# Performance work log

Hardware: AMD Instinct MI355X
Metric: run time of the kernel (lower is better)

Reference implementation:

```python
import jax, jax.numpy as jnp
import numpy as np

B, T, Q, K, H = 8, 128, 64, 64, 4  # batch, agents, q_dim, kv_dim, heads; neighbors n = T-1


def setup_inputs() -> dict:
    key = jax.random.key(0)
    ks = jax.random.split(key, 9)
    s = 0.05
    return {
        "q_x": jax.random.normal(ks[0], (B, T, Q), dtype=jnp.float32),
        "kv_x": jax.random.normal(ks[1], (B, T, T - 1, K), dtype=jnp.float32),
        # nn.Linear weights stored (out_features, in_features), y = x @ W.T + b
        "Wk": jax.random.normal(ks[2], (H * K, K), dtype=jnp.float32) * s,      # tokeys (no bias)
        "Wq": jax.random.normal(ks[3], (H * K, Q), dtype=jnp.float32) * s,      # toqueries (no bias)
        "Wv": jax.random.normal(ks[4], (H * K, K + Q), dtype=jnp.float32) * s,  # tovalues
        "bv": jax.random.normal(ks[5], (H * K,), dtype=jnp.float32) * s,
        "bias": jax.random.uniform(ks[6], (K,), dtype=jnp.float32, minval=-0.1, maxval=0.1),
        "ws": jax.random.normal(ks[7], (K,), dtype=jnp.float32) * s,            # score_proj weight (1, K) -> (K,)
        "bs": jax.random.normal(ks[8], (), dtype=jnp.float32) * s,              # score_proj bias
    }


def reference(q_x, kv_x, Wk, Wq, Wv, bv, bias, ws, bs):
    b, t, n, k = kv_x.shape            # n = t - 1 neighbors
    q = q_x.shape[-1]
    h = Wk.shape[0] // k
    # key / query projections
    keys = jnp.einsum('btnk,ok->btno', kv_x, Wk).reshape(b, t, n, h, k)
    queries = jnp.einsum('btq,oq->bto', q_x, Wq).reshape(b, t, 1, h, k)
    # additive (Bahdanau) score: linear(tanh(keys + queries + bias)) -> scalar per (b,t,n,h)
    score = jnp.einsum('btnhk,k->btnh', jnp.tanh(keys + queries + bias), ws) + bs
    # values from concat(kv, broadcast query features)
    q_exp = jnp.broadcast_to(q_x[:, :, None, :], (b, t, n, q))
    value_input = jnp.concatenate([kv_x, q_exp], axis=-1)      # (b,t,n,k+q)
    values = (jnp.einsum('btnc,oc->btno', value_input, Wv) + bv).reshape(b, t, n, h, k)
    # softmax over neighbors, weighted sum of values
    w = jax.nn.softmax(score, axis=2)                          # (b,t,n,h)
    x = jnp.einsum('btnh,btnhk->bthk', w, values).reshape(b, t, h * k)
    return x
```

## Files before the change

### kernel.cpp

```cpp
#include <hip/hip_runtime.h>
#include <hip/hip_bf16.h>

#define NB 127
#define SCALE 2.885390081777927f

typedef __attribute__((ext_vector_type(8))) short bf16x8;
typedef __attribute__((ext_vector_type(4))) float f32x4;

#define WKP_S  0
#define WVP_S  16384
#define WQP_S  32768
#define WVQP_S 49152
#define WS_NEEDED ((size_t)(4 * 16384 * 2))

__device__ __forceinline__ short bfs(float f) {
  __hip_bfloat16 h = __float2bfloat16(f);
  return __builtin_bit_cast(short, h);
}
__device__ __forceinline__ unsigned packbf2(float a, float b) {
  unsigned lo = (unsigned short)bfs(a);
  unsigned hi = (unsigned short)bfs(b);
  return lo | (hi << 16);
}
__device__ __forceinline__ float b2f(short s) {
  unsigned u = ((unsigned)(unsigned short)s) << 16;
  return __builtin_bit_cast(float, u);
}
__device__ __forceinline__ bf16x8 gath_s(const float* __restrict__ p, float s) {
  float4 a = *(const float4*)p;
  float4 b = *(const float4*)(p + 4);
  bf16x8 f;
  f[0] = bfs(a.x * s); f[1] = bfs(a.y * s); f[2] = bfs(a.z * s); f[3] = bfs(a.w * s);
  f[4] = bfs(b.x * s); f[5] = bfs(b.y * s); f[6] = bfs(b.z * s); f[7] = bfs(b.w * s);
  return f;
}
__device__ __forceinline__ float sigt(float x) {
  return __builtin_amdgcn_rcpf(__builtin_amdgcn_exp2f(x) + 1.f);
}

__global__ __launch_bounds__(256, 2) void
pack_kernel(const float* __restrict__ Wk, const float* __restrict__ Wq,
            const float* __restrict__ Wv, short* __restrict__ dstall)
{
  const int blk = blockIdx.x;
  const int tid = threadIdx.x;
  const int m = blk >> 4, sub = blk & 15;
  const float* src; int stride, off, dsto; float scl;
  if (m == 0)      { src = Wk; stride = 64;  off = 0;  dsto = WKP_S;  scl = SCALE; }
  else if (m == 1) { src = Wv; stride = 128; off = 0;  dsto = WVP_S;  scl = 1.f; }
  else if (m == 2) { src = Wq; stride = 64;  off = 0;  dsto = WQP_S;  scl = SCALE; }
  else             { src = Wv; stride = 128; off = 64; dsto = WVQP_S; scl = 1.f; }
  short* dst = dstall + dsto;
  int i4 = sub * 256 + tid;
  int o = i4 >> 4, c4 = i4 & 15;
  float4 v = ((const float4*)(src + o * stride + off))[c4];
  int k0 = c4 * 4;
  int kt = k0 >> 5, gg = (k0 & 31) >> 3, j0 = k0 & 7;
  int head = o >> 6, nt = (o >> 4) & 3, ol = o & 15;
  int di = ((((head * 4 + nt) * 2 + kt) * 64) + gg * 16 + ol) * 8 + j0;
  *(uint2*)(dst + di) = make_uint2(packbf2(v.x * scl, v.y * scl),
                                   packbf2(v.z * scl, v.w * scl));
}

template <int PREP>
__global__ __launch_bounds__(256, 2) void
rnn_attn_kernel(const float* __restrict__ q_x, const float* __restrict__ kv_x,
                const float* __restrict__ Wk, const float* __restrict__ Wq,
                const float* __restrict__ Wv, const float* __restrict__ bv,
                const float* __restrict__ bias, const float* __restrict__ wsc,
                const short* __restrict__ pack, float* __restrict__ out)
{
  __shared__ __align__(16) unsigned char Atile[128 * 128];
  __shared__ float4 qv_lds[4][4][4];

  const int tid = threadIdx.x;
  const int bt = blockIdx.x;
  const int lane = tid & 63;
  const int head = tid >> 6;
  const int l15 = lane & 15;
  const int g = lane >> 4;

  const float* kv = kv_x + (size_t)bt * (NB * 64);
  #pragma unroll
  for (int i = 0; i < 8; ++i) {
    int idx = i * 256 + tid;
    int row = idx >> 4, c = idx & 15;
    float4 v = (row < NB) ? ((const float4*)kv)[idx] : make_float4(0.f, 0.f, 0.f, 0.f);
    int byte = (row << 7) + (c << 3);
    byte ^= ((row & 7) << 4);
    *(uint2*)(&Atile[byte]) = make_uint2(packbf2(v.x, v.y), packbf2(v.z, v.w));
  }

  f32x4 qq[4];
  {
    bf16x8 qf0 = gath_s(q_x + bt * 64 + g * 8, 1.f);
    bf16x8 qf1 = gath_s(q_x + bt * 64 + 32 + g * 8, 1.f);
    #pragma unroll
    for (int nt = 0; nt < 4; ++nt) {
      bf16x8 wv0, wv1;
      if (PREP) {
        const bf16x8* pv = (const bf16x8*)(pack + WVQP_S);
        wv0 = pv[((head * 4 + nt) * 2 + 0) * 64 + lane];
        wv1 = pv[((head * 4 + nt) * 2 + 1) * 64 + lane];
      } else {
        int o = head * 64 + nt * 16 + l15;
        wv0 = gath_s(Wv + o * 128 + 64 + g * 8, 1.f);
        wv1 = gath_s(Wv + o * 128 + 64 + 32 + g * 8, 1.f);
      }
      float4 bv4 = ((const float4*)(bv + head * 64))[nt * 4 + g];
      f32x4 b = (f32x4){bv4.x, bv4.y, bv4.z, bv4.w};
      b = __builtin_amdgcn_mfma_f32_16x16x32_bf16(wv0, qf0, b, 0, 0, 0);
      b = __builtin_amdgcn_mfma_f32_16x16x32_bf16(wv1, qf1, b, 0, 0, 0);
      if (l15 == 0) qv_lds[head][nt][g] = make_float4(b[0], b[1], b[2], b[3]);
    }
    #pragma unroll
    for (int nt = 0; nt < 4; ++nt) {
      bf16x8 wq0, wq1;
      if (PREP) {
        const bf16x8* pw = (const bf16x8*)(pack + WQP_S);
        wq0 = pw[((head * 4 + nt) * 2 + 0) * 64 + lane];
        wq1 = pw[((head * 4 + nt) * 2 + 1) * 64 + lane];
      } else {
        int o = head * 64 + nt * 16 + l15;
        wq0 = gath_s(Wq + o * 64 + g * 8, SCALE);
        wq1 = gath_s(Wq + o * 64 + 32 + g * 8, SCALE);
      }
      float4 bs4 = ((const float4*)bias)[nt * 4 + g];
      f32x4 a = (f32x4){bs4.x * SCALE, bs4.y * SCALE, bs4.z * SCALE, bs4.w * SCALE};
      a = __builtin_amdgcn_mfma_f32_16x16x32_bf16(wq0, qf0, a, 0, 0, 0);
      a = __builtin_amdgcn_mfma_f32_16x16x32_bf16(wq1, qf1, a, 0, 0, 0);
      qq[nt] = a;
    }
  }

  f32x4 ws4[4];
  bf16x8 bk[4][2];
  #pragma unroll
  for (int nt = 0; nt < 4; ++nt) {
    float4 t = ((const float4*)wsc)[nt * 4 + g];
    ws4[nt] = (f32x4){-2.f * t.x, -2.f * t.y, -2.f * t.z, -2.f * t.w};
    if (PREP) {
      const bf16x8* pw = (const bf16x8*)(pack + WKP_S);
      bk[nt][0] = pw[((head * 4 + nt) * 2 + 0) * 64 + lane];
      bk[nt][1] = pw[((head * 4 + nt) * 2 + 1) * 64 + lane];
    } else {
      int o = head * 64 + nt * 16 + l15;
      bk[nt][0] = gath_s(Wk + o * 64 + g * 8, SCALE);
      bk[nt][1] = gath_s(Wk + o * 64 + 32 + g * 8, SCALE);
    }
  }

  __syncthreads();

  float pvp0[8], pvp1[8], z = 0.f;
  #pragma unroll
  for (int j = 0; j < 8; ++j) { pvp0[j] = 0.f; pvp1[j] = 0.f; }
  #pragma unroll 1
  for (int mt = 0; mt < 8; ++mt) {
    int row = mt * 16 + l15;
    int byte0 = (row << 7) + g * 16;
    int swz = (l15 & 7) << 4;
    bf16x8 a0 = *(const bf16x8*)(&Atile[byte0 ^ swz]);
    bf16x8 a1 = *(const bf16x8*)(&Atile[(byte0 + 64) ^ swz]);
    float pp0, pp1, pp2, pp3;
    {
      f32x4 acc = qq[0];
      acc = __builtin_amdgcn_mfma_f32_16x16x32_bf16(bk[0][0], a0, acc, 0, 0, 0);
      acc = __builtin_amdgcn_mfma_f32_16x16x32_bf16(bk[0][1], a1, acc, 0, 0, 0);
      pp0 = ws4[0][0] * sigt(acc[0]);
      pp0 = fmaf(ws4[0][1], sigt(acc[1]), pp0);
      pp0 = fmaf(ws4[0][2], sigt(acc[2]), pp0);
      pp0 = fmaf(ws4[0][3], sigt(acc[3]), pp0);
    }
    {
      f32x4 acc = qq[1];
      acc = __builtin_amdgcn_mfma_f32_16x16x32_bf16(bk[1][0], a0, acc, 0, 0, 0);
      acc = __builtin_amdgcn_mfma_f32_16x16x32_bf16(bk[1][1], a1, acc, 0, 0, 0);
      pp1 = ws4[1][0] * sigt(acc[0]);
      pp1 = fmaf(ws4[1][1], sigt(acc[1]), pp1);
      pp1 = fmaf(ws4[1][2], sigt(acc[2]), pp1);
      pp1 = fmaf(ws4[1][3], sigt(acc[3]), pp1);
    }
    {
      f32x4 acc = qq[2];
      acc = __builtin_amdgcn_mfma_f32_16x16x32_bf16(bk[2][0], a0, acc, 0, 0, 0);
      acc = __builtin_amdgcn_mfma_f32_16x16x32_bf16(bk[2][1], a1, acc, 0, 0, 0);
      pp2 = ws4[2][0] * sigt(acc[0]);
      pp2 = fmaf(ws4[2][1], sigt(acc[1]), pp2);
      pp2 = fmaf(ws4[2][2], sigt(acc[2]), pp2);
      pp2 = fmaf(ws4[2][3], sigt(acc[3]), pp2);
    }
    {
      f32x4 acc = qq[3];
      acc = __builtin_amdgcn_mfma_f32_16x16x32_bf16(bk[3][0], a0, acc, 0, 0, 0);
      acc = __builtin_amdgcn_mfma_f32_16x16x32_bf16(bk[3][1], a1, acc, 0, 0, 0);
      pp3 = ws4[3][0] * sigt(acc[0]);
      pp3 = fmaf(ws4[3][1], sigt(acc[1]), pp3);
      pp3 = fmaf(ws4[3][2], sigt(acc[2]), pp3);
      pp3 = fmaf(ws4[3][3], sigt(acc[3]), pp3);
    }
    float p = (pp0 + pp1) + (pp2 + pp3);
    p += __shfl_xor(p, 16);
    p += __shfl_xor(p, 32);
    float e = __expf(p);
    if (mt == 7 && l15 == 15) e = 0.f;
    z += e;
    #pragma unroll
    for (int j = 0; j < 8; ++j) {
      pvp0[j] = fmaf(e, b2f(a0[j]), pvp0[j]);
      pvp1[j] = fmaf(e, b2f(a1[j]), pvp1[j]);
    }
  }

  z += __shfl_xor(z, 1);
  z += __shfl_xor(z, 2);
  z += __shfl_xor(z, 4);
  z += __shfl_xor(z, 8);
  float rz = __builtin_amdgcn_rcpf(z);

  bf16x8 pa0, pa1;
  #pragma unroll
  for (int j = 0; j < 8; ++j) { pa0[j] = bfs(pvp0[j] * rz); pa1[j] = bfs(pvp1[j] * rz); }

  float tt[4];
  #pragma unroll 2
  for (int nt = 0; nt < 4; ++nt) {
    bf16x8 bw0, bw1;
    if (PREP) {
      const bf16x8* pw = (const bf16x8*)(pack + WVP_S);
      bw0 = pw[((head * 4 + nt) * 2 + 0) * 64 + lane];
      bw1 = pw[((head * 4 + nt) * 2 + 1) * 64 + lane];
    } else {
      int o = head * 64 + nt * 16 + l15;
      bw0 = gath_s(Wv + o * 128 + g * 8, 1.f);
      bw1 = gath_s(Wv + o * 128 + 32 + g * 8, 1.f);
    }
    f32x4 c = (f32x4){0.f, 0.f, 0.f, 0.f};
    c = __builtin_amdgcn_mfma_f32_16x16x32_bf16(pa0, bw0, c, 0, 0, 0);
    c = __builtin_amdgcn_mfma_f32_16x16x32_bf16(pa1, bw1, c, 0, 0, 0);
    float t = (c[0] + c[1]) + (c[2] + c[3]);
    t += __shfl_xor(t, 16);
    t += __shfl_xor(t, 32);
    tt[nt] = t;
  }

  float v = tt[0];
  v = (g == 1) ? tt[1] : v;
  v = (g == 2) ? tt[2] : v;
  v = (g == 3) ? tt[3] : v;
  float qv = ((const float*)&qv_lds[head][g][l15 >> 2])[l15 & 3];
  out[bt * 256 + head * 64 + lane] = v + qv;
}

extern "C" void kernel_launch(void* const* d_in, const int* in_sizes, int n_in,
                              void* d_out, int out_size, void* d_ws, size_t ws_size,
                              hipStream_t stream) {
  const float* q_x  = (const float*)d_in[0];
  const float* kv_x = (const float*)d_in[1];
  const float* Wk   = (const float*)d_in[2];
  const float* Wq   = (const float*)d_in[3];
  const float* Wv   = (const float*)d_in[4];
  const float* bv   = (const float*)d_in[5];
  const float* bias = (const float*)d_in[6];
  const float* wsc  = (const float*)d_in[7];
  float* out = (float*)d_out;
  short* pack = (short*)d_ws;

  if (ws_size >= WS_NEEDED) {
    pack_kernel<<<64, 256, 0, stream>>>(Wk, Wq, Wv, pack);
    rnn_attn_kernel<1><<<1024, 256, 0, stream>>>(q_x, kv_x, Wk, Wq, Wv, bv, bias, wsc, pack, out);
  } else {
    rnn_attn_kernel<0><<<1024, 256, 0, stream>>>(q_x, kv_x, Wk, Wq, Wv, bv, bias, wsc, pack, out);
  }
}
```

Before: 28.00 us.

## Process two rows per block with a register prefetch of the second kv tile

Each block now handles two consecutive (batch, agent) rows, so the grid is halved. It uses two LDS tiles: while the first row is computed, the second row's kv data is already loaded into registers and is written to the second tile afterwards. The goal is to hide global-load latency behind compute inside one block. The cost is twice the LDS, extra live registers for the prefetch buffer, fewer blocks for the hardware to interleave, and weight fragments that are still reloaded for each row.

```diff
diff --git a/kernel.cpp b/kernel.cpp
--- a/kernel.cpp
+++ b/kernel.cpp
@@ -70,186 +70,214 @@
                 const float* __restrict__ bias, const float* __restrict__ wsc,
                 const short* __restrict__ pack, float* __restrict__ out)
 {
-  __shared__ __align__(16) unsigned char Atile[128 * 128];
+  __shared__ __align__(16) unsigned char Atile[2][128 * 128];
   __shared__ float4 qv_lds[4][4][4];
 
   const int tid = threadIdx.x;
-  const int bt = blockIdx.x;
+  const int bt0 = blockIdx.x * 2;
   const int lane = tid & 63;
   const int head = tid >> 6;
   const int l15 = lane & 15;
   const int g = lane >> 4;
 
-  const float* kv = kv_x + (size_t)bt * (NB * 64);
+  auto do_bt = [&](int bt, const unsigned char* __restrict__ tile) {
+    f32x4 qq[4];
+    {
+      bf16x8 qf0 = gath_s(q_x + bt * 64 + g * 8, 1.f);
+      bf16x8 qf1 = gath_s(q_x + bt * 64 + 32 + g * 8, 1.f);
+      #pragma unroll
+      for (int nt = 0; nt < 4; ++nt) {
+        bf16x8 wv0, wv1;
+        if (PREP) {
+          const bf16x8* pv = (const bf16x8*)(pack + WVQP_S);
+          wv0 = pv[((head * 4 + nt) * 2 + 0) * 64 + lane];
+          wv1 = pv[((head * 4 + nt) * 2 + 1) * 64 + lane];
+        } else {
+          int o = head * 64 + nt * 16 + l15;
+          wv0 = gath_s(Wv + o * 128 + 64 + g * 8, 1.f);
+          wv1 = gath_s(Wv + o * 128 + 64 + 32 + g * 8, 1.f);
+        }
+        float4 bv4 = ((const float4*)(bv + head * 64))[nt * 4 + g];
+        f32x4 b = (f32x4){bv4.x, bv4.y, bv4.z, bv4.w};
+        b = __builtin_amdgcn_mfma_f32_16x16x32_bf16(wv0, qf0, b, 0, 0, 0);
+        b = __builtin_amdgcn_mfma_f32_16x16x32_bf16(wv1, qf1, b, 0, 0, 0);
+        if (l15 == 0) qv_lds[head][nt][g] = make_float4(b[0], b[1], b[2], b[3]);
+      }
+      #pragma unroll
+      for (int nt = 0; nt < 4; ++nt) {
+        bf16x8 wq0, wq1;
+        if (PREP) {
+          const bf16x8* pw = (const bf16x8*)(pack + WQP_S);
+          wq0 = pw[((head * 4 + nt) * 2 + 0) * 64 + lane];
+          wq1 = pw[((head * 4 + nt) * 2 + 1) * 64 + lane];
+        } else {
+          int o = head * 64 + nt * 16 + l15;
+          wq0 = gath_s(Wq + o * 64 + g * 8, SCALE);
+          wq1 = gath_s(Wq + o * 64 + 32 + g * 8, SCALE);
+        }
+        float4 bs4 = ((const float4*)bias)[nt * 4 + g];
+        f32x4 a = (f32x4){bs4.x * SCALE, bs4.y * SCALE, bs4.z * SCALE, bs4.w * SCALE};
+        a = __builtin_amdgcn_mfma_f32_16x16x32_bf16(wq0, qf0, a, 0, 0, 0);
+        a = __builtin_amdgcn_mfma_f32_16x16x32_bf16(wq1, qf1, a, 0, 0, 0);
+        qq[nt] = a;
+      }
+    }
+
+    f32x4 ws4[4];
+    bf16x8 bk[4][2];
+    #pragma unroll
+    for (int nt = 0; nt < 4; ++nt) {
+      float4 t = ((const float4*)wsc)[nt * 4 + g];
+      ws4[nt] = (f32x4){-2.f * t.x, -2.f * t.y, -2.f * t.z, -2.f * t.w};
+      if (PREP) {
+        const bf16x8* pw = (const bf16x8*)(pack + WKP_S);
+        bk[nt][0] = pw[((head * 4 + nt) * 2 + 0) * 64 + lane];
+        bk[nt][1] = pw[((head * 4 + nt) * 2 + 1) * 64 + lane];
+      } else {
+        int o = head * 64 + nt * 16 + l15;
+        bk[nt][0] = gath_s(Wk + o * 64 + g * 8, SCALE);
+        bk[nt][1] = gath_s(Wk + o * 64 + 32 + g * 8, SCALE);
+      }
+    }
+
+    float pvp0[8], pvp1[8], z = 0.f;
+    #pragma unroll
+    for (int j = 0; j < 8; ++j) { pvp0[j] = 0.f; pvp1[j] = 0.f; }
+    #pragma unroll 1
+    for (int mt = 0; mt < 8; ++mt) {
+      int row = mt * 16 + l15;
+      int byte0 = (row << 7) + g * 16;
+      int swz = (l15 & 7) << 4;
+      bf16x8 a0 = *(const bf16x8*)(tile + (byte0 ^ swz));
+      bf16x8 a1 = *(const bf16x8*)(tile + ((byte0 + 64) ^ swz));
+      float pp0, pp1, pp2, pp3;
+      {
+        f32x4 acc = qq[0];
+        acc = __builtin_amdgcn_mfma_f32_16x16x32_bf16(bk[0][0], a0, acc, 0, 0, 0);
+        acc = __builtin_amdgcn_mfma_f32_16x16x32_bf16(bk[0][1], a1, acc, 0, 0, 0);
+        pp0 = ws4[0][0] * sigt(acc[0]);
+        pp0 = fmaf(ws4[0][1], sigt(acc[1]), pp0);
+        pp0 = fmaf(ws4[0][2], sigt(acc[2]), pp0);
+        pp0 = fmaf(ws4[0][3], sigt(acc[3]), pp0);
+      }
+      {
+        f32x4 acc = qq[1];
+        acc = __builtin_amdgcn_mfma_f32_16x16x32_bf16(bk[1][0], a0, acc, 0, 0, 0);
+        acc = __builtin_amdgcn_mfma_f32_16x16x32_bf16(bk[1][1], a1, acc, 0, 0, 0);
+        pp1 = ws4[1][0] * sigt(acc[0]);
+        pp1 = fmaf(ws4[1][1], sigt(acc[1]), pp1);
+        pp1 = fmaf(ws4[1][2], sigt(acc[2]), pp1);
+        pp1 = fmaf(ws4[1][3], sigt(acc[3]), pp1);
+      }
+      {
+        f32x4 acc = qq[2];
+        acc = __builtin_amdgcn_mfma_f32_16x16x32_bf16(bk[2][0], a0, acc, 0, 0, 0);
+        acc = __builtin_amdgcn_mfma_f32_16x16x32_bf16(bk[2][1], a1, acc, 0, 0, 0);
+        pp2 = ws4[2][0] * sigt(acc[0]);
+        pp2 = fmaf(ws4[2][1], sigt(acc[1]), pp2);
+        pp2 = fmaf(ws4[2][2], sigt(acc[2]), pp2);
+        pp2 = fmaf(ws4[2][3], sigt(acc[3]), pp2);
+      }
+      {
+        f32x4 acc = qq[3];
+        acc = __builtin_amdgcn_mfma_f32_16x16x32_bf16(bk[3][0], a0, acc, 0, 0, 0);
+        acc = __builtin_amdgcn_mfma_f32_16x16x32_bf16(bk[3][1], a1, acc, 0, 0, 0);
+        pp3 = ws4[3][0] * sigt(acc[0]);
+        pp3 = fmaf(ws4[3][1], sigt(acc[1]), pp3);
+        pp3 = fmaf(ws4[3][2], sigt(acc[2]), pp3);
+        pp3 = fmaf(ws4[3][3], sigt(acc[3]), pp3);
+      }
+      float p = (pp0 + pp1) + (pp2 + pp3);
+      p += __shfl_xor(p, 16);
+      p += __shfl_xor(p, 32);
+      float e = __expf(p);
+      if (mt == 7 && l15 == 15) e = 0.f;
+      z += e;
+      #pragma unroll
+      for (int j = 0; j < 8; ++j) {
+        pvp0[j] = fmaf(e, b2f(a0[j]), pvp0[j]);
+        pvp1[j] = fmaf(e, b2f(a1[j]), pvp1[j]);
+      }
+    }
+
+    z += __shfl_xor(z, 1);
+    z += __shfl_xor(z, 2);
+    z += __shfl_xor(z, 4);
+    z += __shfl_xor(z, 8);
+    float rz = __builtin_amdgcn_rcpf(z);
+
+    bf16x8 pa0, pa1;
+    #pragma unroll
+    for (int j = 0; j < 8; ++j) { pa0[j] = bfs(pvp0[j] * rz); pa1[j] = bfs(pvp1[j] * rz); }
+
+    float tt[4];
+    #pragma unroll 2
+    for (int nt = 0; nt < 4; ++nt) {
+      bf16x8 bw0, bw1;
+      if (PREP) {
+        const bf16x8* pw = (const bf16x8*)(pack + WVP_S);
+        bw0 = pw[((head * 4 + nt) * 2 + 0) * 64 + lane];
+        bw1 = pw[((head * 4 + nt) * 2 + 1) * 64 + lane];
+      } else {
+        int o = head * 64 + nt * 16 + l15;
+        bw0 = gath_s(Wv + o * 128 + g * 8, 1.f);
+        bw1 = gath_s(Wv + o * 128 + 32 + g * 8, 1.f);
+      }
+      f32x4 c = (f32x4){0.f, 0.f, 0.f, 0.f};
+      c = __builtin_amdgcn_mfma_f32_16x16x32_bf16(pa0, bw0, c, 0, 0, 0);
+      c = __builtin_amdgcn_mfma_f32_16x16x32_bf16(pa1, bw1, c, 0, 0, 0);
+      float t = (c[0] + c[1]) + (c[2] + c[3]);
+      t += __shfl_xor(t, 16);
+      t += __shfl_xor(t, 32);
+      tt[nt] = t;
+    }
+
+    float v = tt[0];
+    v = (g == 1) ? tt[1] : v;
+    v = (g == 2) ? tt[2] : v;
+    v = (g == 3) ? tt[3] : v;
+    float qv = ((const float*)&qv_lds[head][g][l15 >> 2])[l15 & 3];
+    out[bt * 256 + head * 64 + lane] = v + qv;
+  };
+
+  {
+    const float* kv = kv_x + (size_t)bt0 * (NB * 64);
+    #pragma unroll
+    for (int i = 0; i < 8; ++i) {
+      int idx = i * 256 + tid;
+      int row = idx >> 4, c = idx & 15;
+      float4 v = (row < NB) ? ((const float4*)kv)[idx] : make_float4(0.f, 0.f, 0.f, 0.f);
+      int byte = ((row << 7) + (c << 3)) ^ ((row & 7) << 4);
+      *(uint2*)(&Atile[0][byte]) = make_uint2(packbf2(v.x, v.y), packbf2(v.z, v.w));
+    }
+  }
+
+  float4 pf[8];
+  {
+    const float* kv = kv_x + (size_t)(bt0 + 1) * (NB * 64);
+    #pragma unroll
+    for (int i = 0; i < 8; ++i) {
+      int idx = i * 256 + tid;
+      int row = idx >> 4;
+      pf[i] = (row < NB) ? ((const float4*)kv)[idx] : make_float4(0.f, 0.f, 0.f, 0.f);
+    }
+  }
+
+  __syncthreads();
+
+  do_bt(bt0, &Atile[0][0]);
+
   #pragma unroll
   for (int i = 0; i < 8; ++i) {
     int idx = i * 256 + tid;
     int row = idx >> 4, c = idx & 15;
-    float4 v = (row < NB) ? ((const float4*)kv)[idx] : make_float4(0.f, 0.f, 0.f, 0.f);
-    int byte = (row << 7) + (c << 3);
-    byte ^= ((row & 7) << 4);
-    *(uint2*)(&Atile[byte]) = make_uint2(packbf2(v.x, v.y), packbf2(v.z, v.w));
+    int byte = ((row << 7) + (c << 3)) ^ ((row & 7) << 4);
+    *(uint2*)(&Atile[1][byte]) = make_uint2(packbf2(pf[i].x, pf[i].y),
+                                            packbf2(pf[i].z, pf[i].w));
   }
-
-  f32x4 qq[4];
-  {
-    bf16x8 qf0 = gath_s(q_x + bt * 64 + g * 8, 1.f);
-    bf16x8 qf1 = gath_s(q_x + bt * 64 + 32 + g * 8, 1.f);
-    #pragma unroll
-    for (int nt = 0; nt < 4; ++nt) {
-      bf16x8 wv0, wv1;
-      if (PREP) {
-        const bf16x8* pv = (const bf16x8*)(pack + WVQP_S);
-        wv0 = pv[((head * 4 + nt) * 2 + 0) * 64 + lane];
-        wv1 = pv[((head * 4 + nt) * 2 + 1) * 64 + lane];
-      } else {
-        int o = head * 64 + nt * 16 + l15;
-        wv0 = gath_s(Wv + o * 128 + 64 + g * 8, 1.f);
-        wv1 = gath_s(Wv + o * 128 + 64 + 32 + g * 8, 1.f);
-      }
-      float4 bv4 = ((const float4*)(bv + head * 64))[nt * 4 + g];
-      f32x4 b = (f32x4){bv4.x, bv4.y, bv4.z, bv4.w};
-      b = __builtin_amdgcn_mfma_f32_16x16x32_bf16(wv0, qf0, b, 0, 0, 0);
-      b = __builtin_amdgcn_mfma_f32_16x16x32_bf16(wv1, qf1, b, 0, 0, 0);
-      if (l15 == 0) qv_lds[head][nt][g] = make_float4(b[0], b[1], b[2], b[3]);
-    }
-    #pragma unroll
-    for (int nt = 0; nt < 4; ++nt) {
-      bf16x8 wq0, wq1;
-      if (PREP) {
-        const bf16x8* pw = (const bf16x8*)(pack + WQP_S);
-        wq0 = pw[((head * 4 + nt) * 2 + 0) * 64 + lane];
-        wq1 = pw[((head * 4 + nt) * 2 + 1) * 64 + lane];
-      } else {
-        int o = head * 64 + nt * 16 + l15;
-        wq0 = gath_s(Wq + o * 64 + g * 8, SCALE);
-        wq1 = gath_s(Wq + o * 64 + 32 + g * 8, SCALE);
-      }
-      float4 bs4 = ((const float4*)bias)[nt * 4 + g];
-      f32x4 a = (f32x4){bs4.x * SCALE, bs4.y * SCALE, bs4.z * SCALE, bs4.w * SCALE};
-      a = __builtin_amdgcn_mfma_f32_16x16x32_bf16(wq0, qf0, a, 0, 0, 0);
-      a = __builtin_amdgcn_mfma_f32_16x16x32_bf16(wq1, qf1, a, 0, 0, 0);
-      qq[nt] = a;
-    }
-  }
-
-  f32x4 ws4[4];
-  bf16x8 bk[4][2];
-  #pragma unroll
-  for (int nt = 0; nt < 4; ++nt) {
-    float4 t = ((const float4*)wsc)[nt * 4 + g];
-    ws4[nt] = (f32x4){-2.f * t.x, -2.f * t.y, -2.f * t.z, -2.f * t.w};
-    if (PREP) {
-      const bf16x8* pw = (const bf16x8*)(pack + WKP_S);
-      bk[nt][0] = pw[((head * 4 + nt) * 2 + 0) * 64 + lane];
-      bk[nt][1] = pw[((head * 4 + nt) * 2 + 1) * 64 + lane];
-    } else {
-      int o = head * 64 + nt * 16 + l15;
-      bk[nt][0] = gath_s(Wk + o * 64 + g * 8, SCALE);
-      bk[nt][1] = gath_s(Wk + o * 64 + 32 + g * 8, SCALE);
-    }
-  }
-
   __syncthreads();
 
-  float pvp0[8], pvp1[8], z = 0.f;
-  #pragma unroll
-  for (int j = 0; j < 8; ++j) { pvp0[j] = 0.f; pvp1[j] = 0.f; }
-  #pragma unroll 1
-  for (int mt = 0; mt < 8; ++mt) {
-    int row = mt * 16 + l15;
-    int byte0 = (row << 7) + g * 16;
-    int swz = (l15 & 7) << 4;
-    bf16x8 a0 = *(const bf16x8*)(&Atile[byte0 ^ swz]);
-    bf16x8 a1 = *(const bf16x8*)(&Atile[(byte0 + 64) ^ swz]);
-    float pp0, pp1, pp2, pp3;
-    {
-      f32x4 acc = qq[0];
-      acc = __builtin_amdgcn_mfma_f32_16x16x32_bf16(bk[0][0], a0, acc, 0, 0, 0);
-      acc = __builtin_amdgcn_mfma_f32_16x16x32_bf16(bk[0][1], a1, acc, 0, 0, 0);
-      pp0 = ws4[0][0] * sigt(acc[0]);
-      pp0 = fmaf(ws4[0][1], sigt(acc[1]), pp0);
-      pp0 = fmaf(ws4[0][2], sigt(acc[2]), pp0);
-      pp0 = fmaf(ws4[0][3], sigt(acc[3]), pp0);
-    }
-    {
-      f32x4 acc = qq[1];
-      acc = __builtin_amdgcn_mfma_f32_16x16x32_bf16(bk[1][0], a0, acc, 0, 0, 0);
-      acc = __builtin_amdgcn_mfma_f32_16x16x32_bf16(bk[1][1], a1, acc, 0, 0, 0);
-      pp1 = ws4[1][0] * sigt(acc[0]);
-      pp1 = fmaf(ws4[1][1], sigt(acc[1]), pp1);
-      pp1 = fmaf(ws4[1][2], sigt(acc[2]), pp1);
-      pp1 = fmaf(ws4[1][3], sigt(acc[3]), pp1);
-    }
-    {
-      f32x4 acc = qq[2];
-      acc = __builtin_amdgcn_mfma_f32_16x16x32_bf16(bk[2][0], a0, acc, 0, 0, 0);
-      acc = __builtin_amdgcn_mfma_f32_16x16x32_bf16(bk[2][1], a1, acc, 0, 0, 0);
-      pp2 = ws4[2][0] * sigt(acc[0]);
-      pp2 = fmaf(ws4[2][1], sigt(acc[1]), pp2);
-      pp2 = fmaf(ws4[2][2], sigt(acc[2]), pp2);
-      pp2 = fmaf(ws4[2][3], sigt(acc[3]), pp2);
-    }
-    {
-      f32x4 acc = qq[3];
-      acc = __builtin_amdgcn_mfma_f32_16x16x32_bf16(bk[3][0], a0, acc, 0, 0, 0);
-      acc = __builtin_amdgcn_mfma_f32_16x16x32_bf16(bk[3][1], a1, acc, 0, 0, 0);
-      pp3 = ws4[3][0] * sigt(acc[0]);
-      pp3 = fmaf(ws4[3][1], sigt(acc[1]), pp3);
-      pp3 = fmaf(ws4[3][2], sigt(acc[2]), pp3);
-      pp3 = fmaf(ws4[3][3], sigt(acc[3]), pp3);
-    }
-    float p = (pp0 + pp1) + (pp2 + pp3);
-    p += __shfl_xor(p, 16);
-    p += __shfl_xor(p, 32);
-    float e = __expf(p);
-    if (mt == 7 && l15 == 15) e = 0.f;
-    z += e;
-    #pragma unroll
-    for (int j = 0; j < 8; ++j) {
-      pvp0[j] = fmaf(e, b2f(a0[j]), pvp0[j]);
-      pvp1[j] = fmaf(e, b2f(a1[j]), pvp1[j]);
-    }
-  }
-
-  z += __shfl_xor(z, 1);
-  z += __shfl_xor(z, 2);
-  z += __shfl_xor(z, 4);
-  z += __shfl_xor(z, 8);
-  float rz = __builtin_amdgcn_rcpf(z);
-
-  bf16x8 pa0, pa1;
-  #pragma unroll
-  for (int j = 0; j < 8; ++j) { pa0[j] = bfs(pvp0[j] * rz); pa1[j] = bfs(pvp1[j] * rz); }
-
-  float tt[4];
-  #pragma unroll 2
-  for (int nt = 0; nt < 4; ++nt) {
-    bf16x8 bw0, bw1;
-    if (PREP) {
-      const bf16x8* pw = (const bf16x8*)(pack + WVP_S);
-      bw0 = pw[((head * 4 + nt) * 2 + 0) * 64 + lane];
-      bw1 = pw[((head * 4 + nt) * 2 + 1) * 64 + lane];
-    } else {
-      int o = head * 64 + nt * 16 + l15;
-      bw0 = gath_s(Wv + o * 128 + g * 8, 1.f);
-      bw1 = gath_s(Wv + o * 128 + 32 + g * 8, 1.f);
-    }
-    f32x4 c = (f32x4){0.f, 0.f, 0.f, 0.f};
-    c = __builtin_amdgcn_mfma_f32_16x16x32_bf16(pa0, bw0, c, 0, 0, 0);
-    c = __builtin_amdgcn_mfma_f32_16x16x32_bf16(pa1, bw1, c, 0, 0, 0);
-    float t = (c[0] + c[1]) + (c[2] + c[3]);
-    t += __shfl_xor(t, 16);
-    t += __shfl_xor(t, 32);
-    tt[nt] = t;
-  }
-
-  float v = tt[0];
-  v = (g == 1) ? tt[1] : v;
-  v = (g == 2) ? tt[2] : v;
-  v = (g == 3) ? tt[3] : v;
-  float qv = ((const float*)&qv_lds[head][g][l15 >> 2])[l15 & 3];
-  out[bt * 256 + head * 64 + lane] = v + qv;
+  do_bt(bt0 + 1, &Atile[1][0]);
 }
 
 extern "C" void kernel_launch(void* const* d_in, const int* in_sizes, int n_in,
@@ -268,8 +296,8 @@
 
   if (ws_size >= WS_NEEDED) {
     pack_kernel<<<64, 256, 0, stream>>>(Wk, Wq, Wv, pack);
-    rnn_attn_kernel<1><<<1024, 256, 0, stream>>>(q_x, kv_x, Wk, Wq, Wv, bv, bias, wsc, pack, out);
+    rnn_attn_kernel<1><<<512, 256, 0, stream>>>(q_x, kv_x, Wk, Wq, Wv, bv, bias, wsc, pack, out);
   } else {
-    rnn_attn_kernel<0><<<1024, 256, 0, stream>>>(q_x, kv_x, Wk, Wq, Wv, bv, bias, wsc, pack, out);
+    rnn_attn_kernel<0><<<512, 256, 0, stream>>>(q_x, kv_x, Wk, Wq, Wv, bv, bias, wsc, pack, out);
   }
 }
```

New measurement: 30.36 us. 1.08x slower.
